# Performance work log

Measured on AMD Instinct MI355X. Metric: run time of the kernel, lower is better.

The kernel has to match this reference:

```python
import jax, jax.numpy as jnp
import numpy as np

SIGMA = 1.0  # RBF bandwidth (kernel passed to HSIC.__init__)


def _rbf_kernel(A):
    # Gaussian RBF Gram matrix: K_ij = exp(-||a_i - a_j||^2 / (2*sigma^2))
    sq = jnp.sum(A * A, axis=1)                     # [n]
    d2 = sq[:, None] + sq[None, :] - 2.0 * (A @ A.T)  # [n, n] squared dists
    d2 = jnp.maximum(d2, 0.0)
    return jnp.exp(-d2 / (2.0 * SIGMA ** 2))


def setup_inputs() -> dict:
    key = jax.random.key(0)
    kx, ky = jax.random.split(key)
    n, d = 4096, 512
    X = jax.random.normal(kx, (n, d), dtype=jnp.float32)
    Y = jax.random.normal(ky, (n, d), dtype=jnp.float32)
    return {"X": X, "Y": Y}


def reference(X, Y):
    n = X.shape[0]
    K = _rbf_kernel(X)                      # [n, n]
    L = _rbf_kernel(Y)                      # [n, n]
    H = jnp.eye(n, dtype=X.dtype) - 1.0 / n  # centering matrix
    KH = K @ H                              # [n, n]
    LH = L @ H                              # [n, n]
    KHLH = KH @ LH                          # [n, n]
    return jnp.trace(KHLH) / (n ** 2)
```

## Files before the change

### kernel.cpp

```cpp
#include <hip/hip_runtime.h>

#define NROW 4096
#define DIM  512
#define NT   32

using short8 = __attribute__((ext_vector_type(8))) short;
using f32x4  = __attribute__((ext_vector_type(4))) float;

__device__ __forceinline__ unsigned short f2bf(float f) {
  unsigned u = __float_as_uint(f);
  u += 0x7FFFu + ((u >> 16) & 1u);
  return (unsigned short)(u >> 16);
}
__device__ __forceinline__ float bf2f(unsigned short s) {
  return __uint_as_float(((unsigned)s) << 16);
}

__global__ void __launch_bounds__(256) prep_kernel(
    const float* __restrict__ X, const float* __restrict__ Y,
    unsigned short* __restrict__ Xb, unsigned short* __restrict__ Yb,
    float* __restrict__ sqx, float* __restrict__ sqy,
    float* __restrict__ acc ) {
  int tid = threadIdx.x;
  if (blockIdx.x == 0) {
    for (int i = tid; i < 2 * NROW + 1; i += 256) acc[i] = 0.f;
  }
  int lane = tid & 63, w = tid >> 6;
  int row = blockIdx.x * 4 + w;

  {
    const float* xr = X + (size_t)row * DIM;
    unsigned short* xo = Xb + (size_t)row * DIM;
    float s = 0.f;
#pragma unroll
    for (int it = 0; it < 2; ++it) {
      int k = it * 256 + lane * 4;
      float4 v = *reinterpret_cast<const float4*>(xr + k);
      ushort4 o;
      o.x = f2bf(v.x); o.y = f2bf(v.y); o.z = f2bf(v.z); o.w = f2bf(v.w);
      float f0 = bf2f(o.x), f1 = bf2f(o.y), f2 = bf2f(o.z), f3 = bf2f(o.w);
      s += f0 * f0 + f1 * f1 + f2 * f2 + f3 * f3;
      *reinterpret_cast<ushort4*>(xo + k) = o;
    }
#pragma unroll
    for (int m = 1; m < 64; m <<= 1) s += __shfl_xor(s, m);
    if (lane == 0) sqx[row] = s;
  }
  {
    const float* yr = Y + (size_t)row * DIM;
    unsigned short* yo = Yb + (size_t)row * DIM;
    float s = 0.f;
#pragma unroll
    for (int it = 0; it < 2; ++it) {
      int k = it * 256 + lane * 4;
      float4 v = *reinterpret_cast<const float4*>(yr + k);
      ushort4 o;
      o.x = f2bf(v.x); o.y = f2bf(v.y); o.z = f2bf(v.z); o.w = f2bf(v.w);
      float f0 = bf2f(o.x), f1 = bf2f(o.y), f2 = bf2f(o.z), f3 = bf2f(o.w);
      s += f0 * f0 + f1 * f1 + f2 * f2 + f3 * f3;
      *reinterpret_cast<ushort4*>(yo + k) = o;
    }
#pragma unroll
    for (int m = 1; m < 64; m <<= 1) s += __shfl_xor(s, m);
    if (lane == 0) sqy[row] = s;
  }
}

__device__ __forceinline__ void stage_tile(unsigned short* lds,
                                           const unsigned short* gbase,
                                           int tid) {
  int w = tid >> 6;
#pragma unroll
  for (int p = 0; p < 4; ++p) {
    int q = p * 256 + tid;
    int r = q >> 3;
    int c = q & 7;
    int cs = c ^ (r & 7);
    const unsigned short* gp = gbase + r * DIM + cs * 8;
    unsigned short* lp = lds + (p * 256 + w * 64) * 8;
    __builtin_amdgcn_global_load_lds(
        (const __attribute__((address_space(1))) void*)gp,
        (__attribute__((address_space(3))) void*)lp, 16, 0, 0);
  }
}

__device__ __forceinline__ void gemm_tiles(const unsigned short* __restrict__ src,
                                           int bi, int bj, int tid,
                                           unsigned short* At, unsigned short* Bt,
                                           f32x4 acc[4][4]) {
  int lane = tid & 63, w = tid >> 6;
  int wr = w >> 1, wc = w & 1;
  int lr = lane & 15, lg = lane >> 4;
  for (int kb = 0; kb < 8; ++kb) {
    stage_tile(At, src + (size_t)(bi * 128) * DIM + kb * 64, tid);
    stage_tile(Bt, src + (size_t)(bj * 128) * DIM + kb * 64, tid);
    __syncthreads();
#pragma unroll
    for (int kk = 0; kk < 2; ++kk) {
      short8 a[4], b[4];
#pragma unroll
      for (int m = 0; m < 4; ++m) {
        int ra = wr * 64 + m * 16 + lr;
        int ca = kk * 4 + lg;
        a[m] = *reinterpret_cast<const short8*>(At + (ra * 8 + (ca ^ (ra & 7))) * 8);
        int rb = wc * 64 + m * 16 + lr;
        b[m] = *reinterpret_cast<const short8*>(Bt + (rb * 8 + (ca ^ (rb & 7))) * 8);
      }
#pragma unroll
      for (int m = 0; m < 4; ++m)
#pragma unroll
        for (int n = 0; n < 4; ++n)
          acc[m][n] = __builtin_amdgcn_mfma_f32_16x16x32_bf16(a[m], b[n], acc[m][n], 0, 0, 0);
    }
    __syncthreads();
  }
}

__global__ void __launch_bounds__(256, 2) gram_kernel(
    const unsigned short* __restrict__ Xb, const unsigned short* __restrict__ Yb,
    const float* __restrict__ sqx, const float* __restrict__ sqy,
    float* __restrict__ rK, float* __restrict__ rL, float* __restrict__ S1) {
  __shared__ unsigned short At[128 * 64];
  __shared__ unsigned short Bt[128 * 64];
  __shared__ float s1buf[4];

  int tid = threadIdx.x;
  int t = blockIdx.x, bi = 0;
  while (t >= NT - bi) { t -= NT - bi; ++bi; }
  int bj = bi + t;

  f32x4 accK[4][4], accL[4][4];
  f32x4 zz = {0.f, 0.f, 0.f, 0.f};
#pragma unroll
  for (int m = 0; m < 4; ++m)
#pragma unroll
    for (int n = 0; n < 4; ++n) { accK[m][n] = zz; accL[m][n] = zz; }

  gemm_tiles(Xb, bi, bj, tid, At, Bt, accK);
  gemm_tiles(Yb, bi, bj, tid, At, Bt, accL);

  int lane = tid & 63, w = tid >> 6;
  int wr = w >> 1, wc = w & 1;
  int lr = lane & 15, lg = lane >> 4;

  float ckx[4] = {0.f, 0.f, 0.f, 0.f};
  float cky[4] = {0.f, 0.f, 0.f, 0.f};
  float sjx[4], sjy[4]; int gj[4];
#pragma unroll
  for (int n = 0; n < 4; ++n) {
    gj[n] = bj * 128 + wc * 64 + n * 16 + lr;
    sjx[n] = sqx[gj[n]];
    sjy[n] = sqy[gj[n]];
  }
  float s1loc = 0.f;
#pragma unroll
  for (int m = 0; m < 4; ++m) {
#pragma unroll
    for (int r = 0; r < 4; ++r) {
      int gi = bi * 128 + wr * 64 + m * 16 + lg * 4 + r;
      float six = sqx[gi], siy = sqy[gi];
      float rowk = 0.f, rowl = 0.f;
#pragma unroll
      for (int n = 0; n < 4; ++n) {
        float gk = accK[m][n][r];
        float gl = accL[m][n][r];
        float kv, lv;
        if (gi == gj[n]) {
          kv = 1.f; lv = 1.f;
        } else {
          kv = __expf(-0.5f * fmaxf(six + sjx[n] - 2.f * gk, 0.f));
          lv = __expf(-0.5f * fmaxf(siy + sjy[n] - 2.f * gl, 0.f));
        }
        s1loc += kv * lv;
        rowk += kv; rowl += lv;
        ckx[n] += kv; cky[n] += lv;
      }
#pragma unroll
      for (int msk = 1; msk < 16; msk <<= 1) {
        rowk += __shfl_xor(rowk, msk);
        rowl += __shfl_xor(rowl, msk);
      }
      if (lr == 0) { atomicAdd(&rK[gi], rowk); atomicAdd(&rL[gi], rowl); }
    }
  }
  if (bi != bj) {
#pragma unroll
    for (int n = 0; n < 4; ++n) {
      float a = ckx[n], b = cky[n];
      a += __shfl_xor(a, 16); a += __shfl_xor(a, 32);
      b += __shfl_xor(b, 16); b += __shfl_xor(b, 32);
      if (lg == 0) { atomicAdd(&rK[gj[n]], a); atomicAdd(&rL[gj[n]], b); }
    }
    s1loc *= 2.f;
  }
#pragma unroll
  for (int msk = 1; msk < 64; msk <<= 1) s1loc += __shfl_xor(s1loc, msk);
  if (lane == 0) s1buf[w] = s1loc;
  __syncthreads();
  if (tid == 0) atomicAdd(S1, s1buf[0] + s1buf[1] + s1buf[2] + s1buf[3]);
}

__global__ void __launch_bounds__(256) finalize_kernel(
    const float* __restrict__ acc, float* __restrict__ out) {
  const float* rK = acc;
  const float* rL = acc + NROW;
  const float* S1 = acc + 2 * NROW;
  int tid = threadIdx.x, lane = tid & 63, w = tid >> 6;
  float sk = 0.f, sl = 0.f, s2 = 0.f;
  for (int i = tid; i < NROW; i += 256) {
    float a = rK[i], b = rL[i];
    sk += a; sl += b; s2 += a * b;
  }
#pragma unroll
  for (int m = 1; m < 64; m <<= 1) {
    sk += __shfl_xor(sk, m);
    sl += __shfl_xor(sl, m);
    s2 += __shfl_xor(s2, m);
  }
  __shared__ float bk[4], bl[4], b2[4];
  if (lane == 0) { bk[w] = sk; bl[w] = sl; b2[w] = s2; }
  __syncthreads();
  if (tid == 0) {
    double SK = (double)bk[0] + bk[1] + bk[2] + bk[3];
    double SL = (double)bl[0] + bl[1] + bl[2] + bl[3];
    double S2 = (double)b2[0] + b2[1] + b2[2] + b2[3];
    double s1 = (double)S1[0];
    double n = (double)NROW;
    out[0] = (float)((s1 - 2.0 * S2 / n + SK * SL / (n * n)) / (n * n));
  }
}

extern "C" void kernel_launch(void* const* d_in, const int* in_sizes, int n_in,
                              void* d_out, int out_size, void* d_ws, size_t ws_size,
                              hipStream_t stream) {
  (void)in_sizes; (void)n_in; (void)out_size; (void)ws_size;
  const float* X = (const float*)d_in[0];
  const float* Y = (const float*)d_in[1];

  unsigned short* Xb = (unsigned short*)d_ws;
  unsigned short* Yb = Xb + (size_t)NROW * DIM;
  float* sqx = (float*)(Yb + (size_t)NROW * DIM);
  float* sqy = sqx + NROW;
  float* acc = sqy + NROW;

  prep_kernel<<<NROW / 4, 256, 0, stream>>>(X, Y, Xb, Yb, sqx, sqy, acc);
  gram_kernel<<<NT * (NT + 1) / 2, 256, 0, stream>>>(Xb, Yb, sqx, sqy,
                                                     acc, acc + NROW, acc + 2 * NROW);
  finalize_kernel<<<1, 256, 0, stream>>>(acc, (float*)d_out);
}
```

Before: 126.4 us.

## Double-buffer LDS tiles with prefetch and remap blocks across XCDs

Replaces the single-buffered K-loop with a two-stage LDS ring, issuing the asynchronous global-to-LDS loads for the next tile (spanning from the X gram into the Y gram) before computing the current tile. This hides load latency and removes one barrier per step. Block indices are permuted so that consecutive tiles land on the same XCD for L2 reuse. Finalize now uses 1024 threads with vector loads. LDS use doubles to 64KB, which may limit occupancy to two blocks per CU.

```diff
diff --git a/kernel.cpp b/kernel.cpp
--- a/kernel.cpp
+++ b/kernel.cpp
@@ -84,35 +84,25 @@
   }
 }
 
-__device__ __forceinline__ void gemm_tiles(const unsigned short* __restrict__ src,
-                                           int bi, int bj, int tid,
-                                           unsigned short* At, unsigned short* Bt,
-                                           f32x4 acc[4][4]) {
-  int lane = tid & 63, w = tid >> 6;
-  int wr = w >> 1, wc = w & 1;
-  int lr = lane & 15, lg = lane >> 4;
-  for (int kb = 0; kb < 8; ++kb) {
-    stage_tile(At, src + (size_t)(bi * 128) * DIM + kb * 64, tid);
-    stage_tile(Bt, src + (size_t)(bj * 128) * DIM + kb * 64, tid);
-    __syncthreads();
-#pragma unroll
-    for (int kk = 0; kk < 2; ++kk) {
-      short8 a[4], b[4];
-#pragma unroll
-      for (int m = 0; m < 4; ++m) {
-        int ra = wr * 64 + m * 16 + lr;
-        int ca = kk * 4 + lg;
-        a[m] = *reinterpret_cast<const short8*>(At + (ra * 8 + (ca ^ (ra & 7))) * 8);
-        int rb = wc * 64 + m * 16 + lr;
-        b[m] = *reinterpret_cast<const short8*>(Bt + (rb * 8 + (ca ^ (rb & 7))) * 8);
-      }
-#pragma unroll
-      for (int m = 0; m < 4; ++m)
-#pragma unroll
-        for (int n = 0; n < 4; ++n)
-          acc[m][n] = __builtin_amdgcn_mfma_f32_16x16x32_bf16(a[m], b[n], acc[m][n], 0, 0, 0);
-    }
-    __syncthreads();
+__device__ __forceinline__ void tile_mfma(const unsigned short* At, const unsigned short* Bt,
+                                          int lr, int lg, int wr, int wc,
+                                          f32x4 acc[4][4]) {
+#pragma unroll
+  for (int kk = 0; kk < 2; ++kk) {
+    short8 a[4], b[4];
+#pragma unroll
+    for (int m = 0; m < 4; ++m) {
+      int ra = wr * 64 + m * 16 + lr;
+      int ca = kk * 4 + lg;
+      a[m] = *reinterpret_cast<const short8*>(At + (ra * 8 + (ca ^ (ra & 7))) * 8);
+      int rb = wc * 64 + m * 16 + lr;
+      b[m] = *reinterpret_cast<const short8*>(Bt + (rb * 8 + (ca ^ (rb & 7))) * 8);
+    }
+#pragma unroll
+    for (int m = 0; m < 4; ++m)
+#pragma unroll
+      for (int n = 0; n < 4; ++n)
+        acc[m][n] = __builtin_amdgcn_mfma_f32_16x16x32_bf16(a[m], b[n], acc[m][n], 0, 0, 0);
   }
 }
 
@@ -120,28 +110,50 @@
     const unsigned short* __restrict__ Xb, const unsigned short* __restrict__ Yb,
     const float* __restrict__ sqx, const float* __restrict__ sqy,
     float* __restrict__ rK, float* __restrict__ rL, float* __restrict__ S1) {
-  __shared__ unsigned short At[128 * 64];
-  __shared__ unsigned short Bt[128 * 64];
+  __shared__ unsigned short lds[2][2][128 * 64];
   __shared__ float s1buf[4];
 
   int tid = threadIdx.x;
-  int t = blockIdx.x, bi = 0;
+  int wg = (blockIdx.x & 7) * 66 + (blockIdx.x >> 3);
+  int t = wg, bi = 0;
   while (t >= NT - bi) { t -= NT - bi; ++bi; }
   int bj = bi + t;
-
-  f32x4 accK[4][4], accL[4][4];
-  f32x4 zz = {0.f, 0.f, 0.f, 0.f};
-#pragma unroll
-  for (int m = 0; m < 4; ++m)
-#pragma unroll
-    for (int n = 0; n < 4; ++n) { accK[m][n] = zz; accL[m][n] = zz; }
-
-  gemm_tiles(Xb, bi, bj, tid, At, Bt, accK);
-  gemm_tiles(Yb, bi, bj, tid, At, Bt, accL);
 
   int lane = tid & 63, w = tid >> 6;
   int wr = w >> 1, wc = w & 1;
   int lr = lane & 15, lg = lane >> 4;
+
+  f32x4 accK[4][4], accL[4][4];
+  f32x4 zz = {0.f, 0.f, 0.f, 0.f};
+#pragma unroll
+  for (int m = 0; m < 4; ++m)
+#pragma unroll
+    for (int n = 0; n < 4; ++n) { accK[m][n] = zz; accL[m][n] = zz; }
+
+  const size_t rowA = (size_t)(bi * 128) * DIM;
+  const size_t rowB = (size_t)(bj * 128) * DIM;
+
+  auto stage_pair = [&](int it) {
+    const unsigned short* src = (it & 8) ? Yb : Xb;
+    int kb = it & 7;
+    stage_tile(lds[it & 1][0], src + rowA + kb * 64, tid);
+    stage_tile(lds[it & 1][1], src + rowB + kb * 64, tid);
+  };
+
+  stage_pair(0);
+  __syncthreads();
+#pragma unroll
+  for (int kb = 0; kb < 8; ++kb) {
+    stage_pair(kb + 1);
+    tile_mfma(lds[kb & 1][0], lds[kb & 1][1], lr, lg, wr, wc, accK);
+    __syncthreads();
+  }
+#pragma unroll
+  for (int kb = 0; kb < 8; ++kb) {
+    if (kb < 7) stage_pair(8 + kb + 1);
+    tile_mfma(lds[kb & 1][0], lds[kb & 1][1], lr, lg, wr, wc, accL);
+    __syncthreads();
+  }
 
   float ckx[4] = {0.f, 0.f, 0.f, 0.f};
   float cky[4] = {0.f, 0.f, 0.f, 0.f};
@@ -200,30 +212,30 @@
   if (tid == 0) atomicAdd(S1, s1buf[0] + s1buf[1] + s1buf[2] + s1buf[3]);
 }
 
-__global__ void __launch_bounds__(256) finalize_kernel(
+__global__ void __launch_bounds__(1024) finalize_kernel(
     const float* __restrict__ acc, float* __restrict__ out) {
   const float* rK = acc;
   const float* rL = acc + NROW;
   const float* S1 = acc + 2 * NROW;
   int tid = threadIdx.x, lane = tid & 63, w = tid >> 6;
-  float sk = 0.f, sl = 0.f, s2 = 0.f;
-  for (int i = tid; i < NROW; i += 256) {
-    float a = rK[i], b = rL[i];
-    sk += a; sl += b; s2 += a * b;
-  }
+  float4 a = reinterpret_cast<const float4*>(rK)[tid];
+  float4 b = reinterpret_cast<const float4*>(rL)[tid];
+  float sk = a.x + a.y + a.z + a.w;
+  float sl = b.x + b.y + b.z + b.w;
+  float s2 = a.x * b.x + a.y * b.y + a.z * b.z + a.w * b.w;
 #pragma unroll
   for (int m = 1; m < 64; m <<= 1) {
     sk += __shfl_xor(sk, m);
     sl += __shfl_xor(sl, m);
     s2 += __shfl_xor(s2, m);
   }
-  __shared__ float bk[4], bl[4], b2[4];
+  __shared__ float bk[16], bl[16], b2[16];
   if (lane == 0) { bk[w] = sk; bl[w] = sl; b2[w] = s2; }
   __syncthreads();
   if (tid == 0) {
-    double SK = (double)bk[0] + bk[1] + bk[2] + bk[3];
-    double SL = (double)bl[0] + bl[1] + bl[2] + bl[3];
-    double S2 = (double)b2[0] + b2[1] + b2[2] + b2[3];
+    double SK = 0.0, SL = 0.0, S2 = 0.0;
+#pragma unroll
+    for (int i = 0; i < 16; ++i) { SK += bk[i]; SL += bl[i]; S2 += b2[i]; }
     double s1 = (double)S1[0];
     double n = (double)NROW;
     out[0] = (float)((s1 - 2.0 * S2 / n + SK * SL / (n * n)) / (n * n));
@@ -246,5 +258,5 @@
   prep_kernel<<<NROW / 4, 256, 0, stream>>>(X, Y, Xb, Yb, sqx, sqy, acc);
   gram_kernel<<<NT * (NT + 1) / 2, 256, 0, stream>>>(Xb, Yb, sqx, sqy,
                                                      acc, acc + NROW, acc + 2 * NROW);
-  finalize_kernel<<<1, 256, 0, stream>>>(acc, (float*)d_out);
-}
+  finalize_kernel<<<1, 1024, 0, stream>>>(acc, (float*)d_out);
+}
```

Result: faster. 116.6 us (-7.7%).
